# Kernel tuning notes

Hardware: AMD Instinct MI355X
Metric: run time of the kernel (lower is better)

The kernel has to match this reference:

```python
import jax, jax.numpy as jnp
import numpy as np

FEATURES = 32
SINE_WINDOW = 65  # must be odd
SAMPLE_RATE = 16000.0


def setup_inputs() -> dict:
    key = jax.random.key(0)
    k_x, k_ph, k_amp, k_freq, k_res = jax.random.split(key, 5)
    B, S, Cin = 4, 16384, 1
    all_chans = Cin * FEATURES
    x = jax.random.normal(k_x, (B, S, Cin), jnp.float32)
    # time base in seconds (realistic for audio sine filters)
    sine_range = jnp.arange(S, dtype=jnp.float32) / SAMPLE_RATE
    phases = jax.random.uniform(k_ph, (all_chans, 1), jnp.float32)
    # lecun_normal on shape (all_chans, 1): std ~ 1/sqrt(fan_in=all_chans)
    scale = 1.0 / np.sqrt(all_chans)
    amplitude = jax.random.normal(k_amp, (all_chans, 1), jnp.float32) * scale
    frequency = jax.random.normal(k_freq, (all_chans, 1), jnp.float32) * scale
    # flax nn.Conv kernel for kernel_size=(1,), groups=1 (Cin==1): shape (1, Cin, FEATURES)
    res_kernel = jax.random.normal(k_res, (1, Cin, FEATURES), jnp.float32) * (1.0 / np.sqrt(Cin))
    return {"x": x, "sine_range": sine_range, "phases": phases,
            "amplitude": amplitude, "frequency": frequency, "res_kernel": res_kernel}


def _forward(x, sine_range, phases, amplitude, frequency, res_kernel):
    F, W = FEATURES, SINE_WINDOW
    B, S, Cin = x.shape
    L = S - W + 1  # final_seq_len
    sr = sine_range[:S]  # [S]

    # im2col on the signal: [B, Cin, S] -> [B, Cin*W, L] (channel-major patch order)
    xp = jax.lax.conv_general_dilated_patches(
        jnp.transpose(x, (0, 2, 1)), (W,), (1,), ((0, 0),))
    xp = jnp.repeat(xp, F, axis=1)  # [B, Cin*W*F, L]

    freq = frequency * 19000.0          # [A,1], A = Cin*F
    ph = phases * (2.0 * jnp.pi)        # [A,1]
    # sines: [A, S] via broadcasting (matches vmap over rows + squeeze)
    sines = amplitude * jnp.sin(freq * (2.0 * jnp.pi) * sr[None, :] + ph)
    # im2col on the generated sines: [1, A, S] -> [1, A*W, L]
    sp = jax.lax.conv_general_dilated_patches(sines[None], (W,), (1,), ((0, 0),))

    conv = xp * sp                                  # [B, Cin*F*W, L]
    conv = conv.reshape(B, F, Cin * W, L).sum(axis=2)  # [B, F, L]
    conv = jnp.transpose(conv, (0, 2, 1))           # [B, L, F]

    # residual 1x1 conv (group count 1 since Cin == 1)
    x_res = jnp.einsum('bsc,cf->bsf', x, res_kernel[0])  # [B, S, F]
    # cropping callable: center-crop residual to L and add
    start = (S - L) // 2
    x_res = jax.lax.dynamic_slice_in_dim(x_res, start, L, axis=1)
    return conv + x_res


def reference(x, sine_range, phases, amplitude, frequency, res_kernel):
    return _forward(x, sine_range, phases, amplitude, frequency, res_kernel)
```

## Files before the change

kernel.cpp:

```cpp
#include <hip/hip_runtime.h>
#include <math.h>

#define S_LEN 16384
#define L_LEN 16320
#define NF 32
#define TWO_PI 6.283185307179586

__global__ __launch_bounds__(256) void sineconv_kernel(
    const float* __restrict__ x, const float* __restrict__ phases,
    const float* __restrict__ amplitude, const float* __restrict__ frequency,
    const float* __restrict__ rk, float* __restrict__ out)
{
    __shared__ double c_nu[NF], c_b0[NF], c_b1[NF], c_b2[NF];
    __shared__ float c_A0[NF], c_A1[NF], c_A2[NF], c_rk[NF];
    __shared__ float xl[132];

    int b = blockIdx.y;
    int l0 = blockIdx.x * 64;
    int t = threadIdx.x;

    for (int idx = t; idx < 130; idx += 256) {
        int s = l0 + idx; if (s >= S_LEN) s = S_LEN - 1;
        xl[idx] = x[b * S_LEN + s];
    }

    if (t < NF) {
        int f = t;
        double fq  = (double)frequency[f] * 19000.0;
        double nu  = fq / 16000.0;
        double om2 = (TWO_PI * 0.5) * nu;
        double ph  = (double)phases[f];
        double amp = (double)amplitude[f];
        double sh  = sin(om2);
        int n0 = 32 - f, n2 = f + 1;
        double R0, R1, R2v;
        if (fabs(sh) > 1e-30) {
            double inv = 1.0 / sh;
            R0  = sin((double)n0 * om2) * inv;
            R1  = sin(32.0 * om2) * inv;
            R2v = sin((double)n2 * om2) * inv;
        } else {
            R0 = n0; R1 = 32.0; R2v = n2;
        }
        c_nu[f] = nu;
        c_b0[f] = ph + nu * (0.5 * (double)(31 - f));
        c_b1[f] = ph + nu * ((double)(32 - f) + 15.5);
        c_b2[f] = ph + nu * (64.0 - 0.5 * (double)f);
        c_A0[f] = (float)(amp * R0);
        c_A1[f] = (float)(amp * R1);
        c_A2[f] = (float)(amp * R2v);
        c_rk[f] = rk[f];
    }
    __syncthreads();

    int f = t & 31;
    double nu = c_nu[f];
    double b0 = c_b0[f], b1 = c_b1[f], b2 = c_b2[f];
    float A0 = c_A0[f], A1 = c_A1[f], A2 = c_A2[f], rkf = c_rk[f];
    int lb = t >> 5;

#pragma unroll
    for (int k = 0; k < 8; ++k) {
        int li = lb + k * 8;
        double lw = (double)(l0 + li);
        double u0 = fma(nu, lw, b0); u0 -= rint(u0);
        double u1 = fma(nu, lw, b1); u1 -= rint(u1);
        double u2 = fma(nu, lw, b2); u2 -= rint(u2);
        float s0 = A0 * sinf((float)u0 * (float)TWO_PI);
        float s1 = A1 * sinf((float)u1 * (float)TWO_PI);
        float s2 = A2 * sinf((float)u2 * (float)TWO_PI);
        float v = xl[li + 2*f] * s0 + xl[li + 2*f + 1] * s1 + xl[li + 2*f + 2] * s2
                + xl[li + 32] * rkf;
        out[((b * L_LEN) + (l0 + li)) * NF + f] = v;
    }
}

extern "C" void kernel_launch(void* const* d_in, const int* in_sizes, int n_in,
                              void* d_out, int out_size, void* d_ws, size_t ws_size,
                              hipStream_t stream) {
    const float* x    = (const float*)d_in[0];
    const float* ph   = (const float*)d_in[2];
    const float* amp  = (const float*)d_in[3];
    const float* freq = (const float*)d_in[4];
    const float* rk   = (const float*)d_in[5];
    float* out = (float*)d_out;

    sineconv_kernel<<<dim3(L_LEN / 64, 4), 256, 0, stream>>>(x, ph, amp, freq, rk, out);
}
```

Measured before the change: 72.03 us.

## Precompute per-block sine phases in setup kernel; use hardware sin/fract in main

Splits the work into a single-block setup kernel and a main kernel. The setup kernel computes the per-feature coefficients and the double-precision phase base for each 64-sample block, and writes them to workspace. The main kernel then evaluates phases in fp32 relative to the block start using v_fract and the native v_sin intrinsic, which removes all per-element double-precision math and the per-block trig setup. The cost is a second kernel launch, a serial single-block prologue, and lower phase and sine accuracy from fp32 and the hardware sin.

```diff
diff --git a/kernel.cpp b/kernel.cpp
--- a/kernel.cpp
+++ b/kernel.cpp
@@ -4,26 +4,17 @@
 #define S_LEN 16384
 #define L_LEN 16320
 #define NF 32
+#define NBLK 255
 #define TWO_PI 6.283185307179586
 
-__global__ __launch_bounds__(256) void sineconv_kernel(
-    const float* __restrict__ x, const float* __restrict__ phases,
-    const float* __restrict__ amplitude, const float* __restrict__ frequency,
-    const float* __restrict__ rk, float* __restrict__ out)
+
+__global__ __launch_bounds__(256) void sineconv_setup(
+    const float* __restrict__ phases, const float* __restrict__ amplitude,
+    const float* __restrict__ frequency, const float* __restrict__ rk,
+    float* __restrict__ ws)
 {
-    __shared__ double c_nu[NF], c_b0[NF], c_b1[NF], c_b2[NF];
-    __shared__ float c_A0[NF], c_A1[NF], c_A2[NF], c_rk[NF];
-    __shared__ float xl[132];
-
-    int b = blockIdx.y;
-    int l0 = blockIdx.x * 64;
+    __shared__ double s_nu[NF], s_b0[NF], s_b1[NF], s_b2[NF];
     int t = threadIdx.x;
-
-    for (int idx = t; idx < 130; idx += 256) {
-        int s = l0 + idx; if (s >= S_LEN) s = S_LEN - 1;
-        xl[idx] = x[b * S_LEN + s];
-    }
-
     if (t < NF) {
         int f = t;
         double fq  = (double)frequency[f] * 19000.0;
@@ -42,35 +33,68 @@
         } else {
             R0 = n0; R1 = 32.0; R2v = n2;
         }
-        c_nu[f] = nu;
-        c_b0[f] = ph + nu * (0.5 * (double)(31 - f));
-        c_b1[f] = ph + nu * ((double)(32 - f) + 15.5);
-        c_b2[f] = ph + nu * (64.0 - 0.5 * (double)f);
-        c_A0[f] = (float)(amp * R0);
-        c_A1[f] = (float)(amp * R1);
-        c_A2[f] = (float)(amp * R2v);
-        c_rk[f] = rk[f];
+        s_nu[f] = nu;
+        s_b0[f] = ph + nu * (0.5 * (double)(31 - f));
+        s_b1[f] = ph + nu * ((double)(32 - f) + 15.5);
+        s_b2[f] = ph + nu * (64.0 - 0.5 * (double)f);
+        ws[f]        = (float)nu;
+        ws[32 + f]   = (float)(amp * R0);
+        ws[64 + f]   = (float)(amp * R1);
+        ws[96 + f]   = (float)(amp * R2v);
+        ws[128 + f]  = rk[f];
     }
     __syncthreads();
 
     int f = t & 31;
-    double nu = c_nu[f];
-    double b0 = c_b0[f], b1 = c_b1[f], b2 = c_b2[f];
-    float A0 = c_A0[f], A1 = c_A1[f], A2 = c_A2[f], rkf = c_rk[f];
+    double nu = s_nu[f], b0 = s_b0[f], b1 = s_b1[f], b2 = s_b2[f];
+    for (int i = (t >> 5); i < NBLK; i += 8) {
+        double lw = (double)(i * 64);
+        double u0 = fma(nu, lw, b0); u0 -= rint(u0);
+        double u1 = fma(nu, lw, b1); u1 -= rint(u1);
+        double u2 = fma(nu, lw, b2); u2 -= rint(u2);
+        float* dst = ws + 160 + i * 96;
+        dst[f]      = (float)u0;
+        dst[32 + f] = (float)u1;
+        dst[64 + f] = (float)u2;
+    }
+}
+
+__global__ __launch_bounds__(256) void sineconv_main(
+    const float* __restrict__ x, const float* __restrict__ ws,
+    float* __restrict__ out)
+{
+    __shared__ float xl[128];
+    __shared__ float tab[256];
+
+    int b  = blockIdx.y;
+    int l0 = blockIdx.x * 64;
+    int t  = threadIdx.x;
+
+    if (t < 128) xl[t] = x[b * S_LEN + l0 + t];
+    tab[t] = (t < 160) ? ws[t] : ws[160 + blockIdx.x * 96 + (t - 160)];
+    __syncthreads();
+
+    int f  = t & 31;
     int lb = t >> 5;
+    float nuf = tab[f];
+    float A0  = tab[32 + f], A1 = tab[64 + f], A2 = tab[96 + f];
+    float rkf = tab[128 + f];
+    float u0b = tab[160 + f], u1b = tab[192 + f], u2b = tab[224 + f];
 
 #pragma unroll
     for (int k = 0; k < 8; ++k) {
         int li = lb + k * 8;
-        double lw = (double)(l0 + li);
-        double u0 = fma(nu, lw, b0); u0 -= rint(u0);
-        double u1 = fma(nu, lw, b1); u1 -= rint(u1);
-        double u2 = fma(nu, lw, b2); u2 -= rint(u2);
-        float s0 = A0 * sinf((float)u0 * (float)TWO_PI);
-        float s1 = A1 * sinf((float)u1 * (float)TWO_PI);
-        float s2 = A2 * sinf((float)u2 * (float)TWO_PI);
-        float v = xl[li + 2*f] * s0 + xl[li + 2*f + 1] * s1 + xl[li + 2*f + 2] * s2
-                + xl[li + 32] * rkf;
+        float lif = (float)li;
+        float u0 = __builtin_amdgcn_fractf(fmaf(nuf, lif, u0b));
+        float u1 = __builtin_amdgcn_fractf(fmaf(nuf, lif, u1b));
+        float u2 = __builtin_amdgcn_fractf(fmaf(nuf, lif, u2b));
+        float s0 = A0 * __builtin_amdgcn_sinf(u0);
+        float s1 = A1 * __builtin_amdgcn_sinf(u1);
+        float s2 = A2 * __builtin_amdgcn_sinf(u2);
+        float v = xl[li + 2 * f]     * s0
+                + xl[li + 2 * f + 1] * s1
+                + xl[li + 2 * f + 2] * s2
+                + xl[li + 32]        * rkf;
         out[((b * L_LEN) + (l0 + li)) * NF + f] = v;
     }
 }
@@ -83,7 +107,9 @@
     const float* amp  = (const float*)d_in[3];
     const float* freq = (const float*)d_in[4];
     const float* rk   = (const float*)d_in[5];
+    float* ws  = (float*)d_ws;
     float* out = (float*)d_out;
 
-    sineconv_kernel<<<dim3(L_LEN / 64, 4), 256, 0, stream>>>(x, ph, amp, freq, rk, out);
+    sineconv_setup<<<dim3(1), 256, 0, stream>>>(ph, amp, freq, rk, ws);
+    sineconv_main<<<dim3(NBLK, 4), 256, 0, stream>>>(x, ws, out);
 }
```

Measured after the change: 69.57 us. -3.4%, faster.

## Replace per-element double-precision sines with angle-addition recurrence from per-block table

Applied to the files above, without the earlier changes.

The inner loop no longer computes three fp64 phase reductions and three sinf calls per output. Each block now precomputes per-feature sin/cos coefficients at its base position, and each thread rotates a single sin/cos pair forward by 8 samples using angle addition. The hardware revolution-based sin/cos intrinsics are also used in the setup. This removes most fp64 and transcendental work per output element. In exchange it adds fp32 recurrence drift over 8 steps and slightly lower accuracy in the per-block coefficients.

```diff
diff --git a/kernel.cpp b/kernel.cpp
--- a/kernel.cpp
+++ b/kernel.cpp
@@ -4,74 +4,102 @@
 #define S_LEN 16384
 #define L_LEN 16320
 #define NF 32
-#define TWO_PI 6.283185307179586
+#define NBLK 255
 
-__global__ __launch_bounds__(256) void sineconv_kernel(
+
+__device__ __forceinline__ float sinrev64(double rev) {
+    double u = rev - rint(rev);
+    return __builtin_amdgcn_sinf((float)u);
+}
+__device__ __forceinline__ float cosrev64(double rev) {
+    double u = rev - rint(rev);
+    return __builtin_amdgcn_cosf((float)u);
+}
+
+__global__ __launch_bounds__(256) void sineconv_fused(
     const float* __restrict__ x, const float* __restrict__ phases,
     const float* __restrict__ amplitude, const float* __restrict__ frequency,
     const float* __restrict__ rk, float* __restrict__ out)
 {
-    __shared__ double c_nu[NF], c_b0[NF], c_b1[NF], c_b2[NF];
-    __shared__ float c_A0[NF], c_A1[NF], c_A2[NF], c_rk[NF];
-    __shared__ float xl[132];
+    __shared__ float xl[128];
+    __shared__ float tab[10 * NF];
 
-    int b = blockIdx.y;
+    int b  = blockIdx.y;
     int l0 = blockIdx.x * 64;
-    int t = threadIdx.x;
+    int t  = threadIdx.x;
 
-    for (int idx = t; idx < 130; idx += 256) {
-        int s = l0 + idx; if (s >= S_LEN) s = S_LEN - 1;
-        xl[idx] = x[b * S_LEN + s];
-    }
+    if (t < 128) xl[t] = x[b * S_LEN + l0 + t];
 
     if (t < NF) {
         int f = t;
-        double fq  = (double)frequency[f] * 19000.0;
-        double nu  = fq / 16000.0;
-        double om2 = (TWO_PI * 0.5) * nu;
-        double ph  = (double)phases[f];
-        double amp = (double)amplitude[f];
-        double sh  = sin(om2);
+        double fq   = (double)frequency[f] * 19000.0;
+        double nu   = fq * (1.0 / 16000.0);
+        double hrev = 0.5 * nu;
+        double ph   = (double)phases[f];
+        float  amp  = amplitude[f];
+        float  sh   = sinrev64(hrev);
         int n0 = 32 - f, n2 = f + 1;
-        double R0, R1, R2v;
-        if (fabs(sh) > 1e-30) {
-            double inv = 1.0 / sh;
-            R0  = sin((double)n0 * om2) * inv;
-            R1  = sin(32.0 * om2) * inv;
-            R2v = sin((double)n2 * om2) * inv;
+        float R0, R1, R2;
+        if (fabsf(sh) > 1e-30f) {
+            float inv = 1.0f / sh;
+            R0 = sinrev64((double)n0 * hrev) * inv;
+            R1 = sinrev64(32.0 * hrev) * inv;
+            R2 = sinrev64((double)n2 * hrev) * inv;
         } else {
-            R0 = n0; R1 = 32.0; R2v = n2;
+            R0 = (float)n0; R1 = 32.0f; R2 = (float)n2;
         }
-        c_nu[f] = nu;
-        c_b0[f] = ph + nu * (0.5 * (double)(31 - f));
-        c_b1[f] = ph + nu * ((double)(32 - f) + 15.5);
-        c_b2[f] = ph + nu * (64.0 - 0.5 * (double)f);
-        c_A0[f] = (float)(amp * R0);
-        c_A1[f] = (float)(amp * R1);
-        c_A2[f] = (float)(amp * R2v);
-        c_rk[f] = rk[f];
+        float A0 = amp * R0, A1 = amp * R1, A2 = amp * R2;
+
+        double b0 = ph + nu * (0.5 * (double)(31 - f));
+        double b1 = ph + nu * ((double)(32 - f) + 15.5);
+        double b2 = ph + nu * (64.0 - 0.5 * (double)f);
+        double lw = (double)l0;
+        double u0 = fma(nu, lw, b0); u0 -= rint(u0);
+        double u1 = fma(nu, lw, b1); u1 -= rint(u1);
+        double u2 = fma(nu, lw, b2); u2 -= rint(u2);
+
+        float f0 = (float)u0, f1 = (float)u1, f2 = (float)u2;
+        tab[f]            = (float)nu;
+        tab[NF * 1 + f]   = A0 * __builtin_amdgcn_sinf(f0);
+        tab[NF * 2 + f]   = A0 * __builtin_amdgcn_cosf(f0);
+        tab[NF * 3 + f]   = A1 * __builtin_amdgcn_sinf(f1);
+        tab[NF * 4 + f]   = A1 * __builtin_amdgcn_cosf(f1);
+        tab[NF * 5 + f]   = A2 * __builtin_amdgcn_sinf(f2);
+        tab[NF * 6 + f]   = A2 * __builtin_amdgcn_cosf(f2);
+        tab[NF * 7 + f]   = rk[f];
+        double d8 = 8.0 * nu;
+        tab[NF * 8 + f]   = sinrev64(d8);
+        tab[NF * 9 + f]   = cosrev64(d8);
     }
     __syncthreads();
 
-    int f = t & 31;
-    double nu = c_nu[f];
-    double b0 = c_b0[f], b1 = c_b1[f], b2 = c_b2[f];
-    float A0 = c_A0[f], A1 = c_A1[f], A2 = c_A2[f], rkf = c_rk[f];
+    int f  = t & 31;
     int lb = t >> 5;
+    float nuf = tab[f];
+    float P0 = tab[NF * 1 + f], Q0 = tab[NF * 2 + f];
+    float P1 = tab[NF * 3 + f], Q1 = tab[NF * 4 + f];
+    float P2 = tab[NF * 5 + f], Q2 = tab[NF * 6 + f];
+    float rkf = tab[NF * 7 + f];
+    float sd = tab[NF * 8 + f], cd = tab[NF * 9 + f];
+
+    float u0t = __builtin_amdgcn_fractf(nuf * (float)lb);
+    float st = __builtin_amdgcn_sinf(u0t);
+    float ct = __builtin_amdgcn_cosf(u0t);
 
 #pragma unroll
     for (int k = 0; k < 8; ++k) {
         int li = lb + k * 8;
-        double lw = (double)(l0 + li);
-        double u0 = fma(nu, lw, b0); u0 -= rint(u0);
-        double u1 = fma(nu, lw, b1); u1 -= rint(u1);
-        double u2 = fma(nu, lw, b2); u2 -= rint(u2);
-        float s0 = A0 * sinf((float)u0 * (float)TWO_PI);
-        float s1 = A1 * sinf((float)u1 * (float)TWO_PI);
-        float s2 = A2 * sinf((float)u2 * (float)TWO_PI);
-        float v = xl[li + 2*f] * s0 + xl[li + 2*f + 1] * s1 + xl[li + 2*f + 2] * s2
-                + xl[li + 32] * rkf;
+        float s0 = fmaf(P0, ct, Q0 * st);
+        float s1 = fmaf(P1, ct, Q1 * st);
+        float s2 = fmaf(P2, ct, Q2 * st);
+        float v = xl[li + 2 * f]     * s0
+                + xl[li + 2 * f + 1] * s1
+                + xl[li + 2 * f + 2] * s2
+                + xl[li + 32]        * rkf;
         out[((b * L_LEN) + (l0 + li)) * NF + f] = v;
+        float nst = fmaf(st, cd, ct * sd);
+        float nct = fmaf(ct, cd, -st * sd);
+        st = nst; ct = nct;
     }
 }
 
@@ -85,5 +113,5 @@
     const float* rk   = (const float*)d_in[5];
     float* out = (float*)d_out;
 
-    sineconv_kernel<<<dim3(L_LEN / 64, 4), 256, 0, stream>>>(x, ph, amp, freq, rk, out);
+    sineconv_fused<<<dim3(NBLK, 4), 256, 0, stream>>>(x, ph, amp, freq, rk, out);
 }
```

After: 65.94 us. 1.09x faster.
